# Optimization experiments

Hardware: AMD Instinct MI355X
Metric: run time of the kernel (lower is better)

Reference implementation:

```python
import jax, jax.numpy as jnp
import numpy as np

N_NODES = 30000
N_REL = 8
N_EDGES = 150000
EMB = 128
HID = 128
OUT = 256
HEADS = 4
RANK = 8
SCALE = 1.0
NEG_SLOPE = 0.2
LN_EPS = 1e-5


def setup_inputs():
    key = jax.random.key(0)
    ks = jax.random.split(key, 16)
    def nrm(k, shp, s=0.05):
        return jax.random.normal(k, shp, dtype=jnp.float32) * s
    d2 = HEADS * HID  # conv2 input dim = 512
    return {
        "entity_emb": nrm(ks[0], (N_NODES, EMB)),
        "A1": nrm(ks[1], (N_REL, EMB * RANK)),
        "B1": nrm(ks[2], (N_REL, EMB * RANK)),
        "W1": nrm(ks[3], (HEADS * HID, EMB)),
        "att_l1": nrm(ks[4], (1, HEADS, HID)),
        "att_r1": nrm(ks[5], (1, HEADS, HID)),
        "relb1": jnp.zeros((N_REL, HEADS), jnp.float32),
        "bias1": jnp.zeros((HEADS * HID,), jnp.float32),
        "A2": nrm(ks[6], (N_REL, d2 * RANK)),
        "B2": nrm(ks[7], (N_REL, d2 * RANK)),
        "W2": nrm(ks[8], (OUT, d2)),
        "att_l2": nrm(ks[9], (1, 1, OUT)),
        "att_r2": nrm(ks[10], (1, 1, OUT)),
        "relb2": jnp.zeros((N_REL, 1), jnp.float32),
        "bias2": jnp.zeros((OUT,), jnp.float32),
        "res_W": nrm(ks[11], (OUT, EMB)),
        "res_b": jnp.zeros((OUT,), jnp.float32),
        "ln_g": jnp.ones((OUT,), jnp.float32),
        "ln_b": jnp.zeros((OUT,), jnp.float32),
        "edge_index": jax.random.randint(ks[12], (2, N_EDGES), 0, N_NODES),
        "edge_type": jax.random.randint(ks[13], (N_EDGES,), 0, N_REL),
    }


def _rel_gat_conv(x, A, B, W, att_l, att_r, relb, bias, j_idx, i_idx, etype, heads, out_dim, concat):
    # x: [N,d]; A,B: [R, d*k]; W: [heads*out_dim, d]
    N, d = x.shape
    R = A.shape[0]
    k = RANK
    HC = heads * out_dim
    A3 = A.reshape(R, d, k)
    B3 = B.reshape(R, d, k)
    z_all = x @ W.T  # [N, HC] base linear (shared by z_i and z_j)
    # LoRA low-rank projection per (node, relation): P[n,r] = B_r^T x_n
    P = jnp.einsum('nd,rdk->nrk', x, B3)          # [N,R,k] (small)
    low = P[j_idx, etype]                          # [E,k]
    # Fused LoRA-through-lin: lin(scale*A_r B_r^T x) = scale * low @ (A_r^T W^T)
    M = jnp.einsum('rdk,hd->rkh', A3, W).reshape(R * k, HC)  # [R*k, HC]
    oh = jax.nn.one_hot(etype, R, dtype=x.dtype)   # [E,R]
    low_exp = (oh[:, :, None] * low[:, None, :]).reshape(-1, R * k)  # [E,R*k]
    z_j = (z_all[j_idx] + SCALE * (low_exp @ M)).reshape(-1, heads, out_dim)  # [E,H,C]
    z_i = z_all[i_idx].reshape(-1, heads, out_dim)                            # [E,H,C]
    alpha = (z_i * att_l).sum(-1) + (z_j * att_r).sum(-1) + relb[etype]       # [E,H]
    alpha = jax.nn.leaky_relu(alpha, NEG_SLOPE)
    # per-relation loop => softmax groups are (relation, target node)
    seg = etype * N + i_idx
    n_seg = R * N
    amax = jax.ops.segment_max(alpha, seg, num_segments=n_seg)
    ex = jnp.exp(alpha - amax[seg])
    den = jax.ops.segment_sum(ex, seg, num_segments=n_seg)
    alpha = ex / den[seg]
    msg = z_j * alpha[:, :, None]                  # [E,H,C]
    out = jax.ops.segment_sum(msg, i_idx, num_segments=N)  # [N,H,C]
    out = out.reshape(N, HC) if concat else out.mean(axis=1)
    return out + bias


def _forward(entity_emb, A1, B1, W1, att_l1, att_r1, relb1, bias1,
             A2, B2, W2, att_l2, att_r2, relb2, bias2,
             res_W, res_b, ln_g, ln_b, edge_index, edge_type):
    j_idx, i_idx = edge_index[0], edge_index[1]
    x0 = entity_emb
    x = _rel_gat_conv(x0, A1, B1, W1, att_l1, att_r1, relb1, bias1,
                      j_idx, i_idx, edge_type, HEADS, HID, True)
    x = jax.nn.elu(x)
    x = _rel_gat_conv(x, A2, B2, W2, att_l2, att_r2, relb2, bias2,
                      j_idx, i_idx, edge_type, 1, OUT, False)
    x = x + (x0 @ res_W.T + res_b)
    mu = x.mean(axis=-1, keepdims=True)
    var = ((x - mu) ** 2).mean(axis=-1, keepdims=True)
    return (x - mu) / jnp.sqrt(var + LN_EPS) * ln_g + ln_b


def reference(entity_emb, A1, B1, W1, att_l1, att_r1, relb1, bias1,
              A2, B2, W2, att_l2, att_r2, relb2, bias2,
              res_W, res_b, ln_g, ln_b, edge_index, edge_type):
    return _forward(entity_emb, A1, B1, W1, att_l1, att_r1, relb1, bias1,
                    A2, B2, W2, att_l2, att_r2, relb2, bias2,
                    res_W, res_b, ln_g, ln_b, edge_index, edge_type)
```

## Files before the change

### kernel.cpp

```cpp
#include <hip/hip_runtime.h>
#include <cstddef>

#define NRELS 8
#define EMB 128
#define HID 128
#define OUTD 256
#define HEADS 4
#define RANK 8
#define D2 512
#define KCAT 192
#define NEG_SLOPE 0.2f
#define LN_EPS 1e-5f

typedef short bf16x8 __attribute__((ext_vector_type(8)));
typedef float f32x4 __attribute__((ext_vector_type(4)));

__device__ __forceinline__ unsigned short f2bf(float f) {
  union { float f; unsigned u; } v; v.f = f;
  unsigned u = v.u;
  return (unsigned short)((u + 0x7fffu + ((u >> 16) & 1u)) >> 16);
}
__device__ __forceinline__ float bf2f(unsigned short u) {
  union { unsigned u; float f; } v; v.u = (unsigned)u << 16; return v.f;
}

#define GLOAD16(ldsp, gp) \
  __builtin_amdgcn_global_load_lds((const __attribute__((address_space(1))) unsigned int*)(gp), \
      (__attribute__((address_space(3))) unsigned int*)(ldsp), 16, 0, 0)

template<int ATT, int BIAS, int F32OUT, int PB>
__global__ __launch_bounds__(256) void gemm_tile(const unsigned short* __restrict__ A,
    const unsigned short* __restrict__ B, unsigned short* __restrict__ C,
    float* __restrict__ Cf, const unsigned short* __restrict__ Bp,
    float* __restrict__ Cp, int M, int N, int K, int lda, int aoffc,
    const float* __restrict__ bias, const float* __restrict__ b1p,
    const float* __restrict__ attL, const float* __restrict__ attR,
    float* __restrict__ al, float* __restrict__ ar) {
  __shared__ unsigned short As[128 * 64];
  __shared__ unsigned short Bs[128 * 64];
  __shared__ float pL[2][128];
  __shared__ float pR[2][128];
  const int tid = threadIdx.x;
  const int wave = tid >> 6;
  const int lane = tid & 63;
  const int wm = wave & 1;
  const int wn = wave >> 1;
  const int r16 = lane & 15;
  const int quad = lane >> 4;
  const int bm = blockIdx.x * 128;
  const int srow = lane >> 3;
  const int gcol = ((lane & 7) ^ srow) * 8;

  if (PB && blockIdx.y == (int)gridDim.y - 1) {
    const unsigned short* Ag[4];
#pragma unroll
    for (int g = 0; g < 4; ++g) {
      int r = bm + wave * 32 + g * 8 + srow; if (r >= M) r = M - 1;
      Ag[g] = A + (size_t)r * lda + gcol;
    }
    const unsigned short* Bg[2];
#pragma unroll
    for (int g = 0; g < 2; ++g)
      Bg[g] = Bp + (size_t)(wave * 16 + g * 8 + srow) * K + gcol;
    f32x4 accp[4][2] = {};
    for (int k0 = 0; k0 < K; k0 += 64) {
      __syncthreads();
#pragma unroll
      for (int g = 0; g < 4; ++g) GLOAD16(As + (wave * 32 + g * 8) * 64, Ag[g] + k0);
#pragma unroll
      for (int g = 0; g < 2; ++g) GLOAD16(Bs + (wave * 16 + g * 8) * 64, Bg[g] + k0);
      __syncthreads();
#pragma unroll
      for (int s = 0; s < 2; ++s) {
        const int rs = ((s * 4 + quad) ^ (r16 & 7)) * 8;
        bf16x8 af[4], bfr[2];
#pragma unroll
        for (int mi = 0; mi < 4; ++mi)
          af[mi] = *(const bf16x8*)(As + (wm * 64 + mi * 16 + r16) * 64 + rs);
#pragma unroll
        for (int ni = 0; ni < 2; ++ni)
          bfr[ni] = *(const bf16x8*)(Bs + (wn * 32 + ni * 16 + r16) * 64 + rs);
#pragma unroll
        for (int mi = 0; mi < 4; ++mi)
#pragma unroll
          for (int ni = 0; ni < 2; ++ni)
            accp[mi][ni] = __builtin_amdgcn_mfma_f32_16x16x32_bf16(af[mi], bfr[ni], accp[mi][ni], 0, 0, 0);
      }
    }
#pragma unroll
    for (int mi = 0; mi < 4; ++mi)
#pragma unroll
      for (int ni = 0; ni < 2; ++ni)
#pragma unroll
        for (int r = 0; r < 4; ++r) {
          int row = bm + wm * 64 + mi * 16 + quad * 4 + r;
          if (row < M)
            Cp[(size_t)row * 64 + wn * 32 + ni * 16 + r16] = accp[mi][ni][r];
        }
    return;
  }

  const int bn = blockIdx.y * 128;
  const unsigned short* Abase = A + (size_t)blockIdx.y * aoffc;
  const unsigned short* Ag[4];
  const unsigned short* Bg[4];
#pragma unroll
  for (int g = 0; g < 4; ++g) {
    int r = bm + wave * 32 + g * 8 + srow; if (r >= M) r = M - 1;
    Ag[g] = Abase + (size_t)r * lda + gcol;
    Bg[g] = B + (size_t)(bn + wave * 32 + g * 8 + srow) * K + gcol;
  }
  f32x4 acc[4][4] = {};
  for (int k0 = 0; k0 < K; k0 += 64) {
    __syncthreads();
#pragma unroll
    for (int g = 0; g < 4; ++g) GLOAD16(As + (wave * 32 + g * 8) * 64, Ag[g] + k0);
#pragma unroll
    for (int g = 0; g < 4; ++g) GLOAD16(Bs + (wave * 32 + g * 8) * 64, Bg[g] + k0);
    __syncthreads();
#pragma unroll
    for (int s = 0; s < 2; ++s) {
      const int rs = ((s * 4 + quad) ^ (r16 & 7)) * 8;
      bf16x8 af[4], bfr[4];
#pragma unroll
      for (int mi = 0; mi < 4; ++mi)
        af[mi] = *(const bf16x8*)(As + (wm * 64 + mi * 16 + r16) * 64 + rs);
#pragma unroll
      for (int ni = 0; ni < 4; ++ni)
        bfr[ni] = *(const bf16x8*)(Bs + (wn * 64 + ni * 16 + r16) * 64 + rs);
#pragma unroll
      for (int mi = 0; mi < 4; ++mi)
#pragma unroll
        for (int ni = 0; ni < 4; ++ni)
          acc[mi][ni] = __builtin_amdgcn_mfma_f32_16x16x32_bf16(af[mi], bfr[ni], acc[mi][ni], 0, 0, 0);
    }
  }
  float bcol[4];
  if (BIAS) {
#pragma unroll
    for (int ni = 0; ni < 4; ++ni) {
      int cn = bn + wn * 64 + ni * 16 + r16;
      bcol[ni] = bias[cn];
      if (F32OUT) bcol[ni] += b1p[cn];
    }
  }
#pragma unroll
  for (int mi = 0; mi < 4; ++mi)
#pragma unroll
    for (int ni = 0; ni < 4; ++ni)
#pragma unroll
      for (int r = 0; r < 4; ++r) {
        int row = bm + wm * 64 + mi * 16 + quad * 4 + r;
        if (row < M) {
          float v = acc[mi][ni][r];
          if (BIAS) v += bcol[ni];
          size_t idx = (size_t)row * N + bn + wn * 64 + ni * 16 + r16;
          if (F32OUT) Cf[idx] = v;
          else        C[idx] = f2bf(v);
        }
      }
  if (ATT) {
    float La[4], Ra[4];
#pragma unroll
    for (int ni = 0; ni < 4; ++ni) {
      int cn = bn + wn * 64 + ni * 16 + r16;
      La[ni] = attL[cn]; Ra[ni] = attR[cn];
    }
#pragma unroll
    for (int mi = 0; mi < 4; ++mi)
#pragma unroll
      for (int r = 0; r < 4; ++r) {
        float sl = 0.f, sr = 0.f;
#pragma unroll
        for (int ni = 0; ni < 4; ++ni) {
          sl = fmaf(acc[mi][ni][r], La[ni], sl);
          sr = fmaf(acc[mi][ni][r], Ra[ni], sr);
        }
#pragma unroll
        for (int o = 1; o < 16; o <<= 1) {
          sl += __shfl_xor(sl, o, 64);
          sr += __shfl_xor(sr, o, 64);
        }
        if (r16 == 0) {
          int rl = wm * 64 + mi * 16 + quad * 4 + r;
          pL[wn][rl] = sl; pR[wn][rl] = sr;
        }
      }
    __syncthreads();
    if (tid < 128) {
      int row = bm + tid;
      if (row < M) {
        float sl = pL[0][tid] + pL[1][tid];
        float sr = pR[0][tid] + pR[1][tid];
        if (ATT == 1) {
          al[(size_t)row * 4 + blockIdx.y] = sl;
          ar[(size_t)row * 4 + blockIdx.y] = sr;
        } else {
          al[(size_t)blockIdx.y * M + row] = sl;
          ar[(size_t)blockIdx.y * M + row] = sr;
        }
      }
    }
  }
}

__global__ __launch_bounds__(256) void gemm_abt2(const float* __restrict__ Amat1,
    const float* __restrict__ W1, float* __restrict__ M1o,
    const float* __restrict__ Amat2, const float* __restrict__ W2, float* __restrict__ M2o) {
  const float* A; const float* B; float* C; int N, K, bn;
  if (blockIdx.x < D2 / 64) { A = Amat1; B = W1; C = M1o; N = D2; K = EMB; bn = blockIdx.x * 64; }
  else { A = Amat2; B = W2; C = M2o; N = OUTD; K = D2; bn = (blockIdx.x - D2 / 64) * 64; }
  __shared__ float As[32][64];
  __shared__ float Bs[32][64];
  const int tid = threadIdx.x;
  const int tx = tid & 15;
  const int ty = tid >> 4;
  const int lr = tid & 63;
  const int lq = tid >> 6;
  float acc[4][4] = {};
  for (int k0 = 0; k0 < K; k0 += 32) {
#pragma unroll
    for (int s = 0; s < 2; ++s) {
      const int q = lq + s * 4;
      float4 va = *(const float4*)(A + (size_t)lr * K + k0 + q * 4);
      As[q * 4 + 0][lr] = va.x; As[q * 4 + 1][lr] = va.y;
      As[q * 4 + 2][lr] = va.z; As[q * 4 + 3][lr] = va.w;
      float4 vb = *(const float4*)(B + (size_t)(bn + lr) * K + k0 + q * 4);
      Bs[q * 4 + 0][lr] = vb.x; Bs[q * 4 + 1][lr] = vb.y;
      Bs[q * 4 + 2][lr] = vb.z; Bs[q * 4 + 3][lr] = vb.w;
    }
    __syncthreads();
#pragma unroll
    for (int kk = 0; kk < 32; ++kk) {
      float a[4], b[4];
#pragma unroll
      for (int i2 = 0; i2 < 4; ++i2) { a[i2] = As[kk][ty * 4 + i2]; b[i2] = Bs[kk][tx * 4 + i2]; }
#pragma unroll
      for (int i2 = 0; i2 < 4; ++i2)
#pragma unroll
        for (int j2 = 0; j2 < 4; ++j2)
          acc[i2][j2] = fmaf(a[i2], b[j2], acc[i2][j2]);
    }
    __syncthreads();
  }
#pragma unroll
  for (int i2 = 0; i2 < 4; ++i2)
#pragma unroll
    for (int j2 = 0; j2 < 4; ++j2)
      C[(size_t)(ty * 4 + i2) * N + bn + tx * 4 + j2] = acc[i2][j2];
}

__global__ void prep_all(const float* __restrict__ x0, const float* __restrict__ W1,
    const float* __restrict__ W2, const float* __restrict__ res_W,
    const float* __restrict__ A1, const float* __restrict__ A2,
    const float* __restrict__ B1, const float* __restrict__ B2,
    unsigned short* __restrict__ x0b, unsigned short* __restrict__ Acat,
    unsigned short* __restrict__ W1b, unsigned short* __restrict__ W2b,
    unsigned short* __restrict__ RWcat,
    float* __restrict__ Amat1, float* __restrict__ Amat2,
    unsigned short* __restrict__ Bmat1b, unsigned short* __restrict__ Bmat2b,
    const int* __restrict__ ii, int* __restrict__ ideg, int* __restrict__ prepos,
    int E, int nx0) {
  int idx = blockIdx.x * 256 + threadIdx.x;
  if (idx < E) { prepos[idx] = atomicAdd(&ideg[ii[idx]], 1); return; } idx -= E;
  if (idx < nx0) { unsigned short b = f2bf(x0[idx]); x0b[idx] = b;
    Acat[(size_t)(idx >> 7) * KCAT + (idx & 127)] = b; return; } idx -= nx0;
  if (idx < D2 * EMB) { W1b[idx] = f2bf(W1[idx]); return; } idx -= D2 * EMB;
  if (idx < OUTD * D2) { W2b[idx] = f2bf(W2[idx]); return; } idx -= OUTD * D2;
  if (idx < OUTD * EMB) { RWcat[(size_t)(idx >> 7) * KCAT + (idx & 127)] = f2bf(res_W[idx]); return; } idx -= OUTD * EMB;
  if (idx < 64 * EMB) { int d = idx % EMB, rk = idx / EMB, k = rk & 7, r = rk >> 3;
    Amat1[idx] = A1[(size_t)r * EMB * RANK + (size_t)d * RANK + k]; return; } idx -= 64 * EMB;
  if (idx < 64 * D2) { int d = idx % D2, rk = idx / D2, k = rk & 7, r = rk >> 3;
    Amat2[idx] = A2[(size_t)r * D2 * RANK + (size_t)d * RANK + k]; return; } idx -= 64 * D2;
  if (idx < 64 * EMB) { int d = idx % EMB, rk = idx / EMB, k = rk & 7, r = rk >> 3;
    Bmat1b[idx] = f2bf(B1[(size_t)r * EMB * RANK + (size_t)d * RANK + k]); return; } idx -= 64 * EMB;
  if (idx < 64 * D2) { int d = idx % D2, rk = idx / D2, k = rk & 7, r = rk >> 3;
    Bmat2b[idx] = f2bf(B2[(size_t)r * D2 * RANK + (size_t)d * RANK + k]); }
}

__global__ void fold_build(const float* __restrict__ M1, const float* __restrict__ M2,
                           const float* __restrict__ attR1, const float* __restrict__ attR2,
                           unsigned short* __restrict__ M1T2, unsigned short* __restrict__ RWcat,
                           float* __restrict__ Matt1, float* __restrict__ Matt2) {
  int idx = blockIdx.x * 256 + threadIdx.x;
  if (idx < 512 * 64) { int c = idx >> 6, rk = idx & 63;
    M1T2[idx] = f2bf(M1[(size_t)rk * D2 + c]); return; } idx -= 512 * 64;
  if (idx < 256 * 64) { int c = idx >> 6, rk = idx & 63;
    RWcat[(size_t)c * KCAT + 128 + rk] = f2bf(M2[(size_t)rk * OUTD + c]); return; } idx -= 256 * 64;
  if (idx < 256) { int h = idx & 3, rk = idx >> 2;
    float s = 0.f;
    for (int c = 0; c < HID; ++c)
      s = fmaf(M1[(size_t)rk * D2 + h * HID + c], attR1[h * HID + c], s);
    Matt1[rk * 4 + h] = s; return; } idx -= 256;
  if (idx < 64) {
    float s = 0.f;
    for (int c = 0; c < OUTD; ++c) s = fmaf(M2[(size_t)idx * OUTD + c], attR2[c], s);
    Matt2[idx] = s; }
}

__global__ __launch_bounds__(1024) void exscan_kernel(const int* __restrict__ deg,
                                                      int* __restrict__ rowstart, int n) {
  __shared__ int wsum[16];
  int t = threadIdx.x;
  int lane = t & 63, wid = t >> 6;
  int carry = 0;
  for (int base = 0; base < n; base += 4096) {
    int i0 = base + t * 4;
    int v0 = 0, v1 = 0, v2 = 0, v3 = 0;
    if (i0 + 3 < n) {
      int4 vv = *(const int4*)(deg + i0);
      v0 = vv.x; v1 = vv.y; v2 = vv.z; v3 = vv.w;
    } else {
      if (i0 < n) v0 = deg[i0];
      if (i0 + 1 < n) v1 = deg[i0 + 1];
      if (i0 + 2 < n) v2 = deg[i0 + 2];
      if (i0 + 3 < n) v3 = deg[i0 + 3];
    }
    int tot = v0 + v1 + v2 + v3;
    int x = tot;
#pragma unroll
    for (int o = 1; o < 64; o <<= 1) {
      int y = __shfl_up(x, o, 64);
      if (lane >= o) x += y;
    }
    if (lane == 63) wsum[wid] = x;
    __syncthreads();
    if (t == 0) {
      int s = carry;
      for (int w2 = 0; w2 < 16; ++w2) { int tmp = wsum[w2]; wsum[w2] = s; s += tmp; }
      carry = s;
    }
    __syncthreads();
    int ex0 = x - tot + wsum[wid];
    if (i0 + 3 < n) {
      int4 ov; ov.x = ex0; ov.y = ex0 + v0; ov.z = ex0 + v0 + v1; ov.w = ex0 + v0 + v1 + v2;
      *(int4*)(rowstart + i0) = ov;
    } else {
      if (i0 < n) rowstart[i0] = ex0;
      if (i0 + 1 < n) rowstart[i0 + 1] = ex0 + v0;
      if (i0 + 2 < n) rowstart[i0 + 2] = ex0 + v0 + v1;
      if (i0 + 3 < n) rowstart[i0 + 3] = ex0 + v0 + v1 + v2;
    }
    __syncthreads();
  }
  if (t == 0) rowstart[n] = carry;
}

__global__ void edge_alpha1(const int* __restrict__ ji, const int* __restrict__ ii,
                            const int* __restrict__ et, const int* __restrict__ rowstart,
                            const int* __restrict__ prepos,
                            const float* __restrict__ P1,
                            const float* __restrict__ al1, const float* __restrict__ ar1,
                            const float* __restrict__ relb1, const float* __restrict__ Matt1,
                            float4* __restrict__ recs1, int E) {
  int e = blockIdx.x * blockDim.x + threadIdx.x;
  if (e >= E) return;
  int j = ji[e], i = ii[e], rt = et[e];
  float4 lo0 = *(const float4*)(P1 + (size_t)j * 64 + rt * 8);
  float4 lo1 = *(const float4*)(P1 + (size_t)j * 64 + rt * 8 + 4);
  float low[RANK] = {lo0.x, lo0.y, lo0.z, lo0.w, lo1.x, lo1.y, lo1.z, lo1.w};
  float4 ali = *(const float4*)(al1 + (size_t)i * 4);
  float4 arj = *(const float4*)(ar1 + (size_t)j * 4);
  float4 rb  = *(const float4*)(relb1 + rt * 4);
  float a0 = ali.x + arj.x + rb.x;
  float a1 = ali.y + arj.y + rb.y;
  float a2 = ali.z + arj.z + rb.z;
  float a3 = ali.w + arj.w + rb.w;
#pragma unroll
  for (int k = 0; k < RANK; ++k) {
    float4 mk = *(const float4*)(Matt1 + ((rt * 8 + k) << 2));
    a0 = fmaf(low[k], mk.x, a0); a1 = fmaf(low[k], mk.y, a1);
    a2 = fmaf(low[k], mk.z, a2); a3 = fmaf(low[k], mk.w, a3);
  }
  a0 = (a0 > 0.f) ? a0 : NEG_SLOPE * a0;
  a1 = (a1 > 0.f) ? a1 : NEG_SLOPE * a1;
  a2 = (a2 > 0.f) ? a2 : NEG_SLOPE * a2;
  a3 = (a3 > 0.f) ? a3 : NEG_SLOPE * a3;
  float e0 = expf(a0), e1 = expf(a1), e2 = expf(a2), e3 = expf(a3);
  float4* rp = recs1 + (size_t)(rowstart[i] + prepos[e]) * 4;
  rp[0] = make_float4(__int_as_float(j), e0, e1, e2);
  rp[1] = make_float4(e3, __int_as_float(rt), low[0], low[1]);
  rp[2] = make_float4(low[2], low[3], low[4], low[5]);
  rp[3] = make_float4(low[6], low[7], 0.f, 0.f);
}

__global__ __launch_bounds__(256) void qden1(const float4* __restrict__ recs1,
    const int* __restrict__ rowstart, unsigned short* __restrict__ Q1b,
    float* __restrict__ rden1, int Nn) {
  const int wid = threadIdx.x >> 6, lane = threadIdx.x & 63;
  const int i = blockIdx.x * 4 + wid;
  if (i >= Nn) return;
  const int rt_mine = lane >> 3, k = lane & 7;
  const int s0 = rowstart[i], deg = rowstart[i + 1] - s0;
  const float* rf = (const float*)recs1;
  float q0 = 0.f, q1 = 0.f, q2 = 0.f, q3 = 0.f;
  float d0 = 0.f, d1 = 0.f, d2 = 0.f, d3 = 0.f;
  float4 a0 = {}, a1 = {};
  float lw = 0.f;
  if (deg > 0) {
    a0 = recs1[(size_t)s0 * 4]; a1 = recs1[(size_t)s0 * 4 + 1];
    lw = rf[(size_t)s0 * 16 + 6 + k];
  }
  for (int p = 0; p < deg; ++p) {
    float4 b0 = a0, b1 = a1; float lwn = lw;
    if (p + 1 < deg) {
      b0 = recs1[(size_t)(s0 + p + 1) * 4]; b1 = recs1[(size_t)(s0 + p + 1) * 4 + 1];
      lwn = rf[(size_t)(s0 + p + 1) * 16 + 6 + k];
    }
    int rt = __float_as_int(a1.y);
    if (rt == rt_mine) {
      q0 = fmaf(a0.y, lw, q0); q1 = fmaf(a0.z, lw, q1);
      q2 = fmaf(a0.w, lw, q2); q3 = fmaf(a1.x, lw, q3);
      d0 += a0.y; d1 += a0.z; d2 += a0.w; d3 += a1.x;
    }
    a0 = b0; a1 = b1; lw = lwn;
  }
  float r0 = (d0 > 0.f) ? 1.f / d0 : 0.f;
  float r1 = (d1 > 0.f) ? 1.f / d1 : 0.f;
  float r2 = (d2 > 0.f) ? 1.f / d2 : 0.f;
  float r3 = (d3 > 0.f) ? 1.f / d3 : 0.f;
  size_t qb = (size_t)i * 256;
  Q1b[qb + lane]       = f2bf(q0 * r0);
  Q1b[qb + 64 + lane]  = f2bf(q1 * r1);
  Q1b[qb + 128 + lane] = f2bf(q2 * r2);
  Q1b[qb + 192 + lane] = f2bf(q3 * r3);
  if (k == 0) {
    size_t db = (size_t)i * 32;
    rden1[db + rt_mine]      = r0;
    rden1[db + 8 + rt_mine]  = r1;
    rden1[db + 16 + rt_mine] = r2;
    rden1[db + 24 + rt_mine] = r3;
  }
}

__global__ __launch_bounds__(256) void node_agg1_lite(const float4* __restrict__ recs1,
    const int* __restrict__ rowstart, const unsigned short* __restrict__ z1b,
    const unsigned short* __restrict__ L1b, const float* __restrict__ rden1,
    unsigned short* __restrict__ h1out, int Nn) {
  const int wid = threadIdx.x >> 6;
  const int lane = threadIdx.x & 63;
  const int i = blockIdx.x * 4 + wid;
  if (i >= Nn) return;
  __shared__ float denS[4][32];
  if (lane < 32) denS[wid][lane] = rden1[(size_t)i * 32 + lane];
  const int s0 = rowstart[i];
  const int deg = rowstart[i + 1] - s0;
  const int c0 = lane * 8;
  const float* rf = (const float*)recs1;
  const int hb = (lane >> 4) << 3;
  float acc[8] = {};
  float4 r0 = {}, r1 = {}, r2 = {};
  float2 g0 = {}, g1 = {}, g2 = {};
  uint4 za = {}, zb = {};
  if (deg > 0) { r0 = recs1[(size_t)s0 * 4]; g0 = *(const float2*)(rf + (size_t)s0 * 16 + 4);
    za = *(const uint4*)(z1b + (size_t)__float_as_int(r0.x) * D2 + c0); }
  if (deg > 1) { r1 = recs1[(size_t)(s0 + 1) * 4]; g1 = *(const float2*)(rf + (size_t)(s0 + 1) * 16 + 4);
    zb = *(const uint4*)(z1b + (size_t)__float_as_int(r1.x) * D2 + c0); }
  if (deg > 2) { r2 = recs1[(size_t)(s0 + 2) * 4]; g2 = *(const float2*)(rf + (size_t)(s0 + 2) * 16 + 4); }
  for (int p = 0; p < deg; ++p) {
    float4 r3 = r2; float2 g3 = g2; uint4 zn = zb;
    if (p + 3 < deg) { r3 = recs1[(size_t)(s0 + p + 3) * 4];
                       g3 = *(const float2*)(rf + (size_t)(s0 + p + 3) * 16 + 4); }
    if (p + 2 < deg) zn = *(const uint4*)(z1b + (size_t)__float_as_int(r2.x) * D2 + c0);
    int rt = __float_as_int(g0.y);
    float wlo = (lane & 16) ? r0.z : r0.y;
    float whi = (lane & 16) ? g0.x : r0.w;
    float wt = ((lane & 32) ? whi : wlo) * denS[wid][hb + rt];
    acc[0] = fmaf(wt, bf2f((unsigned short)(za.x & 0xffff)), acc[0]);
    acc[1] = fmaf(wt, bf2f((unsigned short)(za.x >> 16)), acc[1]);
    acc[2] = fmaf(wt, bf2f((unsigned short)(za.y & 0xffff)), acc[2]);
    acc[3] = fmaf(wt, bf2f((unsigned short)(za.y >> 16)), acc[3]);
    acc[4] = fmaf(wt, bf2f((unsigned short)(za.z & 0xffff)), acc[4]);
    acc[5] = fmaf(wt, bf2f((unsigned short)(za.z >> 16)), acc[5]);
    acc[6] = fmaf(wt, bf2f((unsigned short)(za.w & 0xffff)), acc[6]);
    acc[7] = fmaf(wt, bf2f((unsigned short)(za.w >> 16)), acc[7]);
    r0 = r1; g0 = g1; r1 = r2; g1 = g2; r2 = r3; g2 = g3; za = zb; zb = zn;
  }
  uint4 lv = *(const uint4*)(L1b + (size_t)i * D2 + c0);
  unsigned lw[4] = {lv.x, lv.y, lv.z, lv.w};
  unsigned ov[4];
#pragma unroll
  for (int q = 0; q < 4; ++q) {
    float e0 = acc[2 * q]     + bf2f((unsigned short)(lw[q] & 0xffff));
    float e1 = acc[2 * q + 1] + bf2f((unsigned short)(lw[q] >> 16));
    e0 = e0 > 0.f ? e0 : expm1f(e0);
    e1 = e1 > 0.f ? e1 : expm1f(e1);
    ov[q] = (unsigned)f2bf(e0) | ((unsigned)f2bf(e1) << 16);
  }
  *(uint4*)(h1out + (size_t)i * D2 + c0) = make_uint4(ov[0], ov[1], ov[2], ov[3]);
}

__global__ void edge_alpha2(const int* __restrict__ ji, const int* __restrict__ ii,
                            const int* __restrict__ et, const int* __restrict__ rowstart,
                            const int* __restrict__ prepos,
                            const float* __restrict__ P2,
                            const float* __restrict__ al2, const float* __restrict__ ar2,
                            const float* __restrict__ relb2, const float* __restrict__ Matt2,
                            float4* __restrict__ recs2, int E, int Nn) {
  int e = blockIdx.x * blockDim.x + threadIdx.x;
  if (e >= E) return;
  int j = ji[e], i = ii[e], rt = et[e];
  float4 lo0 = *(const float4*)(P2 + (size_t)j * 64 + rt * 8);
  float4 lo1 = *(const float4*)(P2 + (size_t)j * 64 + rt * 8 + 4);
  float low[RANK] = {lo0.x, lo0.y, lo0.z, lo0.w, lo1.x, lo1.y, lo1.z, lo1.w};
  float a = al2[i] + al2[(size_t)Nn + i] + ar2[j] + ar2[(size_t)Nn + j] + relb2[rt];
#pragma unroll
  for (int k = 0; k < RANK; ++k) a = fmaf(low[k], Matt2[rt * RANK + k], a);
  a = (a > 0.f) ? a : NEG_SLOPE * a;
  float ex = expf(a);
  float4* rp = recs2 + (size_t)(rowstart[i] + prepos[e]) * 3;
  rp[0] = make_float4(__int_as_float(j), __int_as_float(rt), ex, low[0]);
  rp[1] = make_float4(low[1], low[2], low[3], low[4]);
  rp[2] = make_float4(low[5], low[6], low[7], 0.f);
}

__global__ __launch_bounds__(256) void qden2(const float4* __restrict__ recs2,
    const int* __restrict__ rowstart, unsigned short* __restrict__ Acat,
    float* __restrict__ rden2, int Nn) {
  const int wid = threadIdx.x >> 6, lane = threadIdx.x & 63;
  const int i = blockIdx.x * 4 + wid;
  if (i >= Nn) return;
  const int rt_mine = lane >> 3, k = lane & 7;
  const int s0 = rowstart[i], deg = rowstart[i + 1] - s0;
  const float* rf = (const float*)recs2;
  float q = 0.f, d = 0.f;
  float4 a0 = {}; float lw = 0.f;
  if (deg > 0) { a0 = recs2[(size_t)s0 * 3]; lw = rf[(size_t)s0 * 12 + 3 + k]; }
  for (int p = 0; p < deg; ++p) {
    float4 b0 = a0; float lwn = lw;
    if (p + 1 < deg) {
      b0 = recs2[(size_t)(s0 + p + 1) * 3];
      lwn = rf[(size_t)(s0 + p + 1) * 12 + 3 + k];
    }
    int rt = __float_as_int(a0.y);
    if (rt == rt_mine) { q = fmaf(a0.z, lw, q); d += a0.z; }
    a0 = b0; lw = lwn;
  }
  float rd = (d > 0.f) ? 1.f / d : 0.f;
  Acat[(size_t)i * KCAT + 128 + lane] = f2bf(q * rd);
  if (k == 0) rden2[(size_t)i * 8 + rt_mine] = rd;
}

__global__ __launch_bounds__(256) void node_agg2_lite(const float4* __restrict__ recs2,
    const int* __restrict__ rowstart, const unsigned short* __restrict__ z2b,
    const float* __restrict__ rden2, const float* __restrict__ o2,
    const float* __restrict__ ln_g, const float* __restrict__ ln_b,
    float* __restrict__ y, int Nn) {
  const int wid = threadIdx.x >> 6;
  const int lane = threadIdx.x & 63;
  const int i = blockIdx.x * 4 + wid;
  if (i >= Nn) return;
  __shared__ float denS[4][NRELS];
  if (lane < NRELS) denS[wid][lane] = rden2[(size_t)i * 8 + lane];
  const int s0 = rowstart[i];
  const int deg = rowstart[i + 1] - s0;
  const int c0 = lane * 4;
  float acc[4] = {};
  float4 r0 = {}, r1 = {}, r2 = {};
  uint2 za = make_uint2(0u, 0u), zb = make_uint2(0u, 0u);
  if (deg > 0) { r0 = recs2[(size_t)s0 * 3];
    za = *(const uint2*)(z2b + (size_t)__float_as_int(r0.x) * OUTD + c0); }
  if (deg > 1) { r1 = recs2[(size_t)(s0 + 1) * 3];
    zb = *(const uint2*)(z2b + (size_t)__float_as_int(r1.x) * OUTD + c0); }
  if (deg > 2) r2 = recs2[(size_t)(s0 + 2) * 3];
  for (int p = 0; p < deg; ++p) {
    float4 r3 = r2;
    uint2 zn = zb;
    if (p + 3 < deg) r3 = recs2[(size_t)(s0 + p + 3) * 3];
    if (p + 2 < deg)
      zn = *(const uint2*)(z2b + (size_t)__float_as_int(r2.x) * OUTD + c0);
    int rt = __float_as_int(r0.y);
    float wt = r0.z * denS[wid][rt];
    acc[0] = fmaf(wt, bf2f((unsigned short)(za.x & 0xffff)), acc[0]);
    acc[1] = fmaf(wt, bf2f((unsigned short)(za.x >> 16)), acc[1]);
    acc[2] = fmaf(wt, bf2f((unsigned short)(za.y & 0xffff)), acc[2]);
    acc[3] = fmaf(wt, bf2f((unsigned short)(za.y >> 16)), acc[3]);
    r0 = r1; r1 = r2; r2 = r3; za = zb; zb = zn;
  }
  float4 rsv = *(const float4*)(o2 + (size_t)i * OUTD + c0);
  float vv[4];
  vv[0] = acc[0] + rsv.x;
  vv[1] = acc[1] + rsv.y;
  vv[2] = acc[2] + rsv.z;
  vv[3] = acc[3] + rsv.w;
  float s = vv[0] + vv[1] + vv[2] + vv[3];
  for (int o = 32; o > 0; o >>= 1) s += __shfl_xor(s, o, 64);
  float mu = s * (1.f / OUTD);
  float q = 0.f;
#pragma unroll
  for (int k = 0; k < 4; ++k) { float d = vv[k] - mu; q += d * d; }
  for (int o = 32; o > 0; o >>= 1) q += __shfl_xor(q, o, 64);
  float rstd = rsqrtf(q * (1.f / OUTD) + LN_EPS);
  float4 g = *(const float4*)(ln_g + c0);
  float4 bb = *(const float4*)(ln_b + c0);
  float4 ov;
  ov.x = (vv[0] - mu) * rstd * g.x + bb.x;
  ov.y = (vv[1] - mu) * rstd * g.y + bb.y;
  ov.z = (vv[2] - mu) * rstd * g.z + bb.z;
  ov.w = (vv[3] - mu) * rstd * g.w + bb.w;
  *(float4*)(y + (size_t)i * OUTD + c0) = ov;
}

extern "C" void kernel_launch(void* const* d_in, const int* in_sizes, int n_in,
                              void* d_out, int out_size, void* d_ws, size_t ws_size,
                              hipStream_t stream) {
  const float* x0     = (const float*)d_in[0];
  const float* A1     = (const float*)d_in[1];
  const float* B1     = (const float*)d_in[2];
  const float* W1     = (const float*)d_in[3];
  const float* attL1  = (const float*)d_in[4];
  const float* attR1  = (const float*)d_in[5];
  const float* relb1  = (const float*)d_in[6];
  const float* bias1  = (const float*)d_in[7];
  const float* A2     = (const float*)d_in[8];
  const float* B2     = (const float*)d_in[9];
  const float* W2     = (const float*)d_in[10];
  const float* attL2  = (const float*)d_in[11];
  const float* attR2  = (const float*)d_in[12];
  const float* relb2  = (const float*)d_in[13];
  const float* bias2  = (const float*)d_in[14];
  const float* res_W  = (const float*)d_in[15];
  const float* res_b  = (const float*)d_in[16];
  const float* ln_g   = (const float*)d_in[17];
  const float* ln_b   = (const float*)d_in[18];
  const int*   eidx   = (const int*)d_in[19];
  const int*   etype  = (const int*)d_in[20];
  float* out = (float*)d_out;

  const int Nn = in_sizes[0] / EMB;
  const int E  = in_sizes[20];
  const int* ji = eidx;
  const int* ii = eidx + E;

  float* w = (float*)d_ws;
  size_t off = 0;
  float* o2    = w + off; off += (size_t)Nn * OUTD;
  float* P1    = w + off; off += (size_t)Nn * 64;
  float* P2    = w + off; off += (size_t)Nn * 64;
  float* M1    = w + off; off += 64 * D2;
  float* M2    = w + off; off += 64 * OUTD;
  float* Amat1 = w + off; off += 64 * EMB;
  float* Amat2 = w + off; off += 64 * D2;
  float* Matt1 = w + off; off += 64 * 4;
  float* Matt2 = w + off; off += 64;
  float* al1   = w + off; off += (size_t)Nn * 4;
  float* ar1   = w + off; off += (size_t)Nn * 4;
  float* al2   = w + off; off += (size_t)Nn * 2;
  float* ar2   = w + off; off += (size_t)Nn * 2;
  float* rden1 = w + off; off += (size_t)Nn * 32;
  float* rden2 = w + off; off += (size_t)Nn * 8;
  float4* recs1 = (float4*)(w + off); off += (size_t)E * 16;
  float4* recs2 = (float4*)(w + off); off += (size_t)E * 12;
  unsigned short* z1b    = (unsigned short*)(w + off); off += (size_t)Nn * D2 / 2;
  unsigned short* z2b    = (unsigned short*)(w + off); off += (size_t)Nn * OUTD / 2;
  unsigned short* x0b    = (unsigned short*)(w + off); off += (size_t)Nn * EMB / 2;
  unsigned short* h1b    = (unsigned short*)(w + off); off += (size_t)Nn * D2 / 2;
  unsigned short* W1b    = (unsigned short*)(w + off); off += (size_t)D2 * EMB / 2;
  unsigned short* W2b    = (unsigned short*)(w + off); off += (size_t)OUTD * D2 / 2;
  unsigned short* Bmat1b = (unsigned short*)(w + off); off += (size_t)64 * EMB / 2;
  unsigned short* Bmat2b = (unsigned short*)(w + off); off += (size_t)64 * D2 / 2;
  unsigned short* Acat   = (unsigned short*)(w + off); off += (size_t)Nn * KCAT / 2;
  unsigned short* RWcat  = (unsigned short*)(w + off); off += (size_t)OUTD * KCAT / 2;
  unsigned short* M1T2   = (unsigned short*)(w + off); off += (size_t)512 * 64 / 2;
  int* ideg     = (int*)(w + off); off += (size_t)Nn;
  int* prepos   = (int*)(w + off); off += (size_t)E;
  int* rowstart = (int*)(w + off); off += (size_t)Nn + 1;
  (void)ws_size; (void)n_in; (void)out_size;

  unsigned short* Q1b = (unsigned short*)P1;
  unsigned short* L1b = (unsigned short*)o2;

  const int MT128 = (Nn + 127) / 128;
  const int NB4 = (Nn + 3) / 4;

  (void)hipMemsetAsync(ideg, 0, (size_t)Nn * sizeof(int), stream);
  {
    int nx0 = Nn * EMB;
    int total = E + nx0 + D2 * EMB + OUTD * D2 + OUTD * EMB
              + 64 * EMB + 64 * D2 + 64 * EMB + 64 * D2;
    prep_all<<<(total + 255) / 256, 256, 0, stream>>>(x0, W1, W2, res_W, A1, A2, B1, B2,
        x0b, Acat, W1b, W2b, RWcat, Amat1, Amat2, Bmat1b, Bmat2b, ii, ideg, prepos, E, nx0);
  }
  exscan_kernel<<<1, 1024, 0, stream>>>(ideg, rowstart, Nn);

  gemm_abt2<<<dim3(D2 / 64 + OUTD / 64, 1), 256, 0, stream>>>(Amat1, W1, M1, Amat2, W2, M2);
  fold_build<<<(512 * 64 + 256 * 64 + 256 + 64 + 255) / 256, 256, 0, stream>>>(
      M1, M2, attR1, attR2, M1T2, RWcat, Matt1, Matt2);

  gemm_tile<1, 0, 0, 1><<<dim3(MT128, D2 / 128 + 1), 256, 0, stream>>>(x0b, W1b, z1b, nullptr,
      Bmat1b, P1, Nn, D2, EMB, EMB, 0, nullptr, nullptr, attL1, attR1, al1, ar1);

  edge_alpha1<<<(E + 255) / 256, 256, 0, stream>>>(ji, ii, etype, rowstart, prepos, P1,
                                                   al1, ar1, relb1, Matt1, recs1, E);
  qden1<<<NB4, 256, 0, stream>>>(recs1, rowstart, Q1b, rden1, Nn);
  gemm_tile<0, 1, 0, 0><<<dim3(MT128, D2 / 128), 256, 0, stream>>>(Q1b, M1T2, L1b, nullptr,
      nullptr, nullptr, Nn, D2, 64, 256, 64, bias1, nullptr, nullptr, nullptr, nullptr, nullptr);
  node_agg1_lite<<<NB4, 256, 0, stream>>>(recs1, rowstart, z1b, L1b, rden1, h1b, Nn);

  gemm_tile<2, 0, 0, 1><<<dim3(MT128, OUTD / 128 + 1), 256, 0, stream>>>(h1b, W2b, z2b, nullptr,
      Bmat2b, P2, Nn, OUTD, D2, D2, 0, nullptr, nullptr, attL2, attR2, al2, ar2);

  edge_alpha2<<<(E + 255) / 256, 256, 0, stream>>>(ji, ii, etype, rowstart, prepos, P2,
                                                   al2, ar2, relb2, Matt2, recs2, E, Nn);
  qden2<<<NB4, 256, 0, stream>>>(recs2, rowstart, Acat, rden2, Nn);
  gemm_tile<0, 1, 1, 0><<<dim3(MT128, OUTD / 128), 256, 0, stream>>>(Acat, RWcat, nullptr, o2,
      nullptr, nullptr, Nn, OUTD, KCAT, KCAT, 0, bias2, res_b, nullptr, nullptr, nullptr, nullptr);
  node_agg2_lite<<<NB4, 256, 0, stream>>>(recs2, rowstart, z2b, rden2, o2, ln_g, ln_b, out, Nn);
}
```

Measured before the change: 375.8 us.

## Double-buffer GEMM LDS tiles with K-step 32 and async prefetch

```diff
diff --git a/kernel.cpp b/kernel.cpp
--- a/kernel.cpp
+++ b/kernel.cpp
@@ -36,8 +36,8 @@
     const float* __restrict__ bias, const float* __restrict__ b1p,
     const float* __restrict__ attL, const float* __restrict__ attR,
     float* __restrict__ al, float* __restrict__ ar) {
-  __shared__ unsigned short As[128 * 64];
-  __shared__ unsigned short Bs[128 * 64];
+  __shared__ unsigned short As[2][128 * 32];
+  __shared__ unsigned short Bs[2][128 * 32];
   __shared__ float pL[2][128];
   __shared__ float pR[2][128];
   const int tid = threadIdx.x;
@@ -48,44 +48,42 @@
   const int r16 = lane & 15;
   const int quad = lane >> 4;
   const int bm = blockIdx.x * 128;
-  const int srow = lane >> 3;
-  const int gcol = ((lane & 7) ^ srow) * 8;
+  const int lr = lane >> 2;
+  const int lc = ((lane & 3) ^ ((lane >> 3) & 3)) * 8;
+  const int rsw = (quad ^ ((r16 >> 1) & 3)) * 8;
+  int ar0 = bm + wave * 32 + lr;      if (ar0 >= M) ar0 = M - 1;
+  int ar1 = bm + wave * 32 + 16 + lr; if (ar1 >= M) ar1 = M - 1;
 
   if (PB && blockIdx.y == (int)gridDim.y - 1) {
-    const unsigned short* Ag[4];
-#pragma unroll
-    for (int g = 0; g < 4; ++g) {
-      int r = bm + wave * 32 + g * 8 + srow; if (r >= M) r = M - 1;
-      Ag[g] = A + (size_t)r * lda + gcol;
-    }
-    const unsigned short* Bg[2];
-#pragma unroll
-    for (int g = 0; g < 2; ++g)
-      Bg[g] = Bp + (size_t)(wave * 16 + g * 8 + srow) * K + gcol;
+    const unsigned short* Ag0 = A + (size_t)ar0 * lda + lc;
+    const unsigned short* Ag1 = A + (size_t)ar1 * lda + lc;
+    const unsigned short* Bg = Bp + (size_t)(wave * 16 + lr) * K + lc;
     f32x4 accp[4][2] = {};
-    for (int k0 = 0; k0 < K; k0 += 64) {
+    GLOAD16(As[0] + wave * 1024, Ag0);
+    GLOAD16(As[0] + wave * 1024 + 512, Ag1);
+    GLOAD16(Bs[0] + wave * 512, Bg);
+    __syncthreads();
+    int cur = 0;
+    for (int k0 = 0; k0 < K; k0 += 32) {
+      if (k0 + 32 < K) {
+        GLOAD16(As[cur ^ 1] + wave * 1024, Ag0 + k0 + 32);
+        GLOAD16(As[cur ^ 1] + wave * 1024 + 512, Ag1 + k0 + 32);
+        GLOAD16(Bs[cur ^ 1] + wave * 512, Bg + k0 + 32);
+      }
+      bf16x8 af[4], bfr[2];
+#pragma unroll
+      for (int mi = 0; mi < 4; ++mi)
+        af[mi] = *(const bf16x8*)(As[cur] + (wm * 64 + mi * 16 + r16) * 32 + rsw);
+#pragma unroll
+      for (int ni = 0; ni < 2; ++ni)
+        bfr[ni] = *(const bf16x8*)(Bs[cur] + (wn * 32 + ni * 16 + r16) * 32 + rsw);
+#pragma unroll
+      for (int mi = 0; mi < 4; ++mi)
+#pragma unroll
+        for (int ni = 0; ni < 2; ++ni)
+          accp[mi][ni] = __builtin_amdgcn_mfma_f32_16x16x32_bf16(af[mi], bfr[ni], accp[mi][ni], 0, 0, 0);
       __syncthreads();
-#pragma unroll
-      for (int g = 0; g < 4; ++g) GLOAD16(As + (wave * 32 + g * 8) * 64, Ag[g] + k0);
-#pragma unroll
-      for (int g = 0; g < 2; ++g) GLOAD16(Bs + (wave * 16 + g * 8) * 64, Bg[g] + k0);
-      __syncthreads();
-#pragma unroll
-      for (int s = 0; s < 2; ++s) {
-        const int rs = ((s * 4 + quad) ^ (r16 & 7)) * 8;
-        bf16x8 af[4], bfr[2];
-#pragma unroll
-        for (int mi = 0; mi < 4; ++mi)
-          af[mi] = *(const bf16x8*)(As + (wm * 64 + mi * 16 + r16) * 64 + rs);
-#pragma unroll
-        for (int ni = 0; ni < 2; ++ni)
-          bfr[ni] = *(const bf16x8*)(Bs + (wn * 32 + ni * 16 + r16) * 64 + rs);
-#pragma unroll
-        for (int mi = 0; mi < 4; ++mi)
-#pragma unroll
-          for (int ni = 0; ni < 2; ++ni)
-            accp[mi][ni] = __builtin_amdgcn_mfma_f32_16x16x32_bf16(af[mi], bfr[ni], accp[mi][ni], 0, 0, 0);
-      }
+      cur ^= 1;
     }
 #pragma unroll
     for (int mi = 0; mi < 4; ++mi)
@@ -102,38 +100,38 @@
 
   const int bn = blockIdx.y * 128;
   const unsigned short* Abase = A + (size_t)blockIdx.y * aoffc;
-  const unsigned short* Ag[4];
-  const unsigned short* Bg[4];
-#pragma unroll
-  for (int g = 0; g < 4; ++g) {
-    int r = bm + wave * 32 + g * 8 + srow; if (r >= M) r = M - 1;
-    Ag[g] = Abase + (size_t)r * lda + gcol;
-    Bg[g] = B + (size_t)(bn + wave * 32 + g * 8 + srow) * K + gcol;
-  }
+  const unsigned short* Ag0 = Abase + (size_t)ar0 * lda + lc;
+  const unsigned short* Ag1 = Abase + (size_t)ar1 * lda + lc;
+  const unsigned short* Bg0 = B + (size_t)(bn + wave * 32 + lr) * K + lc;
+  const unsigned short* Bg1 = B + (size_t)(bn + wave * 32 + 16 + lr) * K + lc;
   f32x4 acc[4][4] = {};
-  for (int k0 = 0; k0 < K; k0 += 64) {
+  GLOAD16(As[0] + wave * 1024, Ag0);
+  GLOAD16(As[0] + wave * 1024 + 512, Ag1);
+  GLOAD16(Bs[0] + wave * 1024, Bg0);
+  GLOAD16(Bs[0] + wave * 1024 + 512, Bg1);
+  __syncthreads();
+  int cur = 0;
+  for (int k0 = 0; k0 < K; k0 += 32) {
+    if (k0 + 32 < K) {
+      GLOAD16(As[cur ^ 1] + wave * 1024, Ag0 + k0 + 32);
+      GLOAD16(As[cur ^ 1] + wave * 1024 + 512, Ag1 + k0 + 32);
+      GLOAD16(Bs[cur ^ 1] + wave * 1024, Bg0 + k0 + 32);
+      GLOAD16(Bs[cur ^ 1] + wave * 1024 + 512, Bg1 + k0 + 32);
+    }
+    bf16x8 af[4], bfr[4];
+#pragma unroll
+    for (int mi = 0; mi < 4; ++mi)
+      af[mi] = *(const bf16x8*)(As[cur] + (wm * 64 + mi * 16 + r16) * 32 + rsw);
+#pragma unroll
+    for (int ni = 0; ni < 4; ++ni)
+      bfr[ni] = *(const bf16x8*)(Bs[cur] + (wn * 64 + ni * 16 + r16) * 32 + rsw);
+#pragma unroll
+    for (int mi = 0; mi < 4; ++mi)
+#pragma unroll
+      for (int ni = 0; ni < 4; ++ni)
+        acc[mi][ni] = __builtin_amdgcn_mfma_f32_16x16x32_bf16(af[mi], bfr[ni], acc[mi][ni], 0, 0, 0);
     __syncthreads();
-#pragma unroll
-    for (int g = 0; g < 4; ++g) GLOAD16(As + (wave * 32 + g * 8) * 64, Ag[g] + k0);
-#pragma unroll
-    for (int g = 0; g < 4; ++g) GLOAD16(Bs + (wave * 32 + g * 8) * 64, Bg[g] + k0);
-    __syncthreads();
-#pragma unroll
-    for (int s = 0; s < 2; ++s) {
-      const int rs = ((s * 4 + quad) ^ (r16 & 7)) * 8;
-      bf16x8 af[4], bfr[4];
-#pragma unroll
-      for (int mi = 0; mi < 4; ++mi)
-        af[mi] = *(const bf16x8*)(As + (wm * 64 + mi * 16 + r16) * 64 + rs);
-#pragma unroll
-      for (int ni = 0; ni < 4; ++ni)
-        bfr[ni] = *(const bf16x8*)(Bs + (wn * 64 + ni * 16 + r16) * 64 + rs);
-#pragma unroll
-      for (int mi = 0; mi < 4; ++mi)
-#pragma unroll
-        for (int ni = 0; ni < 4; ++ni)
-          acc[mi][ni] = __builtin_amdgcn_mfma_f32_16x16x32_bf16(af[mi], bfr[ni], acc[mi][ni], 0, 0, 0);
-    }
+    cur ^= 1;
   }
   float bcol[4];
   if (BIAS) {
```

Result: faster. 367.5 us (-2.2%).
